# Kernel optimization log

Measured on AMD Instinct MI355X. Metric: run time of the kernel, lower is better.

Reference implementation:

```python
import jax, jax.numpy as jnp
import numpy as np

N, B, S, A, H, E = 8, 8192, 64, 16, 512, 4  # agents, batch, state, action, hidden, heads
D = H // E  # attend_dim


def setup_inputs() -> dict:
    key = jax.random.key(0)
    ks = jax.random.split(key, 12)
    g = lambda k, shape, fan: (jax.random.normal(k, shape, jnp.float32) / np.float32(np.sqrt(fan)))
    return {
        "states": jax.random.normal(ks[0], (N, B, S), jnp.float32),
        "actions": jax.random.normal(ks[1], (N, B, A), jnp.float32),
        # per-agent state encoder (Linear + LeakyReLU)
        "Ws": g(ks[2], (N, S, H), S), "bs": jnp.zeros((N, H), jnp.float32),
        # per-agent state-action encoder
        "Wsa": g(ks[3], (N, S + A, H), S + A), "bsa": jnp.zeros((N, H), jnp.float32),
        # shared per-head extractors (key/selector bias-free, value has bias+LeakyReLU)
        "Wk": g(ks[4], (E, H, D), H),
        "Wsel": g(ks[5], (E, H, D), H),
        "Wv": g(ks[6], (E, H, D), H), "bv": jnp.zeros((E, D), jnp.float32),
        # per-agent critic head (2H -> H -> 1)
        "Wc1": g(ks[7], (N, 2 * H, H), 2 * H), "bc1": jnp.zeros((N, H), jnp.float32),
        "Wc2": g(ks[8], (N, H, 1), H), "bc2": jnp.zeros((N, 1), jnp.float32),
        # per-agent value head (2H -> H -> 1)
        "Wv1": g(ks[9], (N, 2 * H, H), 2 * H), "bv1": jnp.zeros((N, H), jnp.float32),
        "Wv2": g(ks[10], (N, H, 1), H), "bv2": jnp.zeros((N, 1), jnp.float32),
    }


def reference(states, actions, Ws, bs, Wsa, bsa, Wk, Wsel, Wv, bv,
              Wc1, bc1, Wc2, bc2, Wv1, bv1, Wv2, bv2):
    lrelu = jax.nn.leaky_relu  # slope 0.01, matches nn.LeakyReLU default
    # encoders: [N,B,H]
    s_enc = lrelu(jnp.einsum('nbs,nsh->nbh', states, Ws) + bs[:, None, :])
    sa = jnp.concatenate([states, actions], axis=-1)
    sa_enc = lrelu(jnp.einsum('nbi,nih->nbh', sa, Wsa) + bsa[:, None, :])
    # per-head keys/selectors/values: [B,E,N,D]
    keys = jnp.einsum('nbh,ehd->bend', sa_enc, Wk)
    sels = jnp.einsum('nbh,ehd->bend', sa_enc, Wsel)
    vals = lrelu(jnp.einsum('nbh,ehd->bend', sa_enc, Wv) + bv[None, :, None, :])
    # each agent i attends over all agents j (including itself; no mask in source)
    logits = jnp.einsum('beid,bejd->beij', sels, keys) / jnp.float32(np.sqrt(D))
    weights = jax.nn.softmax(logits, axis=-1)
    other = jnp.einsum('beij,bejd->beid', weights, vals)  # [B,E,N,D]
    other = jnp.transpose(other, (2, 0, 1, 3)).reshape(N, B, H)  # heads concat -> [N,B,H]
    critic_in = jnp.concatenate([sa_enc, other], axis=-1)  # [N,B,2H]
    value_in = jnp.concatenate([s_enc, other], axis=-1)
    q = jnp.einsum('nbh,nho->nbo', lrelu(jnp.einsum('nbi,nih->nbh', critic_in, Wc1) + bc1[:, None, :]), Wc2) + bc2[:, None, :]
    v = jnp.einsum('nbh,nho->nbo', lrelu(jnp.einsum('nbi,nih->nbh', value_in, Wv1) + bv1[:, None, :]), Wv2) + bv2[:, None, :]
    return q, v  # each [N,B,1]
```

## Files before the change

### kernel.cpp

```cpp
#include <hip/hip_runtime.h>


#define DEVI __device__ __forceinline__

typedef unsigned short us16;
typedef __bf16 bf16x8 __attribute__((ext_vector_type(8)));
typedef float f32x4 __attribute__((ext_vector_type(4)));
typedef unsigned short u16x8 __attribute__((ext_vector_type(8)));

DEVI us16 f2bf(float f) {
  unsigned u = __builtin_bit_cast(unsigned, f);
  u += 0x7FFFu + ((u >> 16) & 1u);
  return (us16)(u >> 16);
}
DEVI float bf2f(us16 h) {
  unsigned u = ((unsigned)h) << 16;
  return __builtin_bit_cast(float, u);
}
DEVI float lrelu(float v) { return v > 0.f ? v : 0.01f * v; }
DEVI int pk2(float a, float b) { return (int)f2bf(a) | ((int)f2bf(b) << 16); }

DEVI void gload16(const us16* g, us16* l) {
  __builtin_amdgcn_global_load_lds(
      (const __attribute__((address_space(1))) void*)g,
      (__attribute__((address_space(3))) void*)l, 16, 0, 0);
}

__global__ void tconv_k(const float* __restrict__ src, long srcSlice, int K, int O,
                        us16* __restrict__ dst, long dstSlice, int dstRowOff,
                        int ldd, int Kpad)
{
  __shared__ float t[32][33];
  const int s = blockIdx.z;
  const int k0 = blockIdx.x * 32, o0 = blockIdx.y * 32;
  const int lx = threadIdx.x, ly = threadIdx.y;
#pragma unroll
  for (int i = 0; i < 4; i++) {
    int k = k0 + ly + i * 8, o = o0 + lx;
    float v = 0.f;
    if (k < K && o < O) v = src[(long)s * srcSlice + (long)k * O + o];
    t[ly + i * 8][lx] = v;
  }
  __syncthreads();
#pragma unroll
  for (int i = 0; i < 4; i++) {
    int o = o0 + ly + i * 8, k = k0 + lx;
    if (o < O && k < Kpad)
      dst[(long)s * dstSlice + (long)(dstRowOff + o) * ldd + k] = f2bf(t[lx][ly + i * 8]);
  }
}

enum { ASRC_F32 = 2, ASRC_F32_CAT = 3 };

template <int ASRC, int KTOT>
__global__ __launch_bounds__(256, 4)
void enc_gemm_k(const float* __restrict__ Ap, long aSlice,
                const float* __restrict__ A2p, long a2Slice,
                const us16* __restrict__ Btp, long bSlice,
                const float* __restrict__ bias, long biasSlice,
                us16* __restrict__ outB, long outSlice, long outRow)
{
  __shared__ us16 lA[128 * 32];
  __shared__ us16 lB[128 * 32];
  const int tid = threadIdx.x;
  const int z = blockIdx.z;
  const int m0 = blockIdx.x * 128;
  const int n0 = blockIdx.y * 128;
  const int wv = tid >> 6, lane = tid & 63;
  const int wm = (wv >> 1) * 64, wn = (wv & 1) * 64;
  const int fr = lane & 15, fk = (lane >> 4) * 8;
  const int rbase = (lane >> 4) * 4;
  const int grow = tid >> 2, gcol = (tid & 3) * 8;

  f32x4 acc[4][4];
#pragma unroll
  for (int i = 0; i < 4; i++)
#pragma unroll
    for (int j = 0; j < 4; j++) acc[i][j] = f32x4{0.f, 0.f, 0.f, 0.f};

  const us16* bbase = Btp + (long)z * bSlice + (long)n0 * KTOT;

  for (int k0 = 0; k0 < KTOT; k0 += 32) {
    int4 ra0, ra1;
    {
      const int srow = tid >> 1, scol0 = (tid & 1) * 16;
      const int kg = k0 + scol0;
      const float* a = nullptr;
      if constexpr (ASRC == ASRC_F32) {
        a = Ap + (long)z * aSlice + (long)(m0 + srow) * 64 + kg;
      } else {
        if (kg < 64)      a = Ap + (long)z * aSlice + (long)(m0 + srow) * 64 + kg;
        else if (kg < 80) a = A2p + (long)z * a2Slice + (long)(m0 + srow) * 16 + (kg - 64);
      }
      float4 f0, f1, f2, f3;
      if (a) { const float4* ap = (const float4*)a; f0 = ap[0]; f1 = ap[1]; f2 = ap[2]; f3 = ap[3]; }
      else   { f0 = make_float4(0.f, 0.f, 0.f, 0.f); f1 = f0; f2 = f0; f3 = f0; }
      ra0.x = pk2(f0.x, f0.y); ra0.y = pk2(f0.z, f0.w); ra0.z = pk2(f1.x, f1.y); ra0.w = pk2(f1.z, f1.w);
      ra1.x = pk2(f2.x, f2.y); ra1.y = pk2(f2.z, f2.w); ra1.z = pk2(f3.x, f3.y); ra1.w = pk2(f3.z, f3.w);
    }

    __syncthreads();
    {
      const us16* bb = bbase + k0 + gcol;
      gload16(bb + (long)grow * KTOT, &lB[tid * 8]);
      gload16(bb + (long)(64 + grow) * KTOT, &lB[2048 + tid * 8]);
    }
    {
      const int srow = tid >> 1, scol0 = (tid & 1) * 16;
      *(int4*)&lA[srow * 32 + scol0]     = ra0;
      *(int4*)&lA[srow * 32 + scol0 + 8] = ra1;
    }
    __syncthreads();

    bf16x8 af[4], bfg[4];
#pragma unroll
    for (int f = 0; f < 4; f++) af[f]  = *(const bf16x8*)&lA[(wm + f * 16 + fr) * 32 + fk];
#pragma unroll
    for (int f = 0; f < 4; f++) bfg[f] = *(const bf16x8*)&lB[(wn + f * 16 + fr) * 32 + fk];
#pragma unroll
    for (int fm = 0; fm < 4; fm++)
#pragma unroll
      for (int fn = 0; fn < 4; fn++)
        acc[fm][fn] = __builtin_amdgcn_mfma_f32_16x16x32_bf16(af[fm], bfg[fn], acc[fm][fn], 0, 0, 0);
  }

#pragma unroll
  for (int fm = 0; fm < 4; fm++) {
#pragma unroll
    for (int fn = 0; fn < 4; fn++) {
      int col = n0 + wn + fn * 16 + fr;
      float badd = bias[(long)z * biasSlice + col];
      us16* op = outB + (long)z * outSlice + (long)(m0 + wm + fm * 16 + rbase) * outRow + col;
#pragma unroll
      for (int j = 0; j < 4; j++) {
        float v = lrelu(acc[fm][fn][j] + badd);
        op[(long)j * outRow] = f2bf(v);
      }
    }
  }
}

enum { EPI_KSV = 1, EPI_DOT = 2 };

template <bool CAT, int EPI, int KTOT>
__global__ __launch_bounds__(256, 4)
void gemm64_k(const us16* __restrict__ Ap, long aSlice,
              const us16* __restrict__ A2p, long a2Slice,
              const us16* __restrict__ Btp, long bSlice,
              const float* __restrict__ bias,
              us16* __restrict__ outB, long outSlice, long outRow,
              const float* __restrict__ dotW, float* __restrict__ partial)
{
  __shared__ us16 lA[128 * 64];
  __shared__ us16 lB[128 * 64];
  const int tid = threadIdx.x;
  const int z = blockIdx.z;
  const int m0 = blockIdx.x * 128;
  const int n0 = blockIdx.y * 128;
  const int wv = tid >> 6, lane = tid & 63;
  const int wm = (wv >> 1) * 64, wn = (wv & 1) * 64;
  const int fr = lane & 15, fk = (lane >> 4) * 8;
  const int rbase = (lane >> 4) * 4;
  const int xorkey = (fr & 7) << 3;

  f32x4 acc[4][4];
#pragma unroll
  for (int i = 0; i < 4; i++)
#pragma unroll
    for (int j = 0; j < 4; j++) acc[i][j] = f32x4{0.f, 0.f, 0.f, 0.f};

  const us16* bbase = Btp + (long)z * bSlice + (long)n0 * KTOT;

  for (int k0 = 0; k0 < KTOT; k0 += 64) {
    __syncthreads();
#pragma unroll
    for (int i = 0; i < 4; i++) {
      const int c = i * 256 + tid;
      const int r = c >> 3;
      const int col = ((c & 7) ^ (r & 7)) << 3;
      const us16* a;
      if constexpr (!CAT) {
        a = Ap + (long)z * aSlice + (long)(m0 + r) * KTOT + (k0 + col);
      } else {
        const int kg = k0 + col;
        a = (kg < 512) ? Ap  + (long)z * aSlice  + (long)(m0 + r) * 512 + kg
                       : A2p + (long)z * a2Slice + (long)(m0 + r) * 512 + (kg - 512);
      }
      gload16(a, &lA[c * 8]);
    }
#pragma unroll
    for (int i = 0; i < 4; i++) {
      const int c = i * 256 + tid;
      const int r = c >> 3;
      const int col = ((c & 7) ^ (r & 7)) << 3;
      gload16(bbase + (long)r * KTOT + (k0 + col), &lB[c * 8]);
    }
    __syncthreads();

#pragma unroll
    for (int ks = 0; ks < 2; ks++) {
      bf16x8 af[4], bfg[4];
      const int kc = ks * 32 + fk;
#pragma unroll
      for (int f = 0; f < 4; f++)
        af[f]  = *(const bf16x8*)&lA[(wm + f * 16 + fr) * 64 + (kc ^ xorkey)];
#pragma unroll
      for (int f = 0; f < 4; f++)
        bfg[f] = *(const bf16x8*)&lB[(wn + f * 16 + fr) * 64 + (kc ^ xorkey)];
#pragma unroll
      for (int fm = 0; fm < 4; fm++)
#pragma unroll
        for (int fn = 0; fn < 4; fn++)
          acc[fm][fn] = __builtin_amdgcn_mfma_f32_16x16x32_bf16(af[fm], bfg[fn], acc[fm][fn], 0, 0, 0);
    }
  }

  if constexpr (EPI == EPI_DOT) {
    const float* bsl = bias + (long)z * 512;
    const float* wsl = dotW + (long)z * 512;
#pragma unroll
    for (int fm = 0; fm < 4; fm++) {
#pragma unroll
      for (int j = 0; j < 4; j++) {
        float p = 0.f;
#pragma unroll
        for (int fn = 0; fn < 4; fn++) {
          int col = n0 + wn + fn * 16 + fr;
          float v = acc[fm][fn][j] + bsl[col];
          v = lrelu(v);
          p += v * wsl[col];
        }
        p += __shfl_xor(p, 1); p += __shfl_xor(p, 2); p += __shfl_xor(p, 4); p += __shfl_xor(p, 8);
        if (fr == 0) {
          long row = (long)z * 8192 + (m0 + wm + fm * 16 + rbase + j);
          partial[row * 8 + blockIdx.y * 2 + (wv & 1)] = p;
        }
      }
    }
  } else {
#pragma unroll
    for (int fm = 0; fm < 4; fm++) {
#pragma unroll
      for (int fn = 0; fn < 4; fn++) {
        int col = n0 + wn + fn * 16 + fr;
        float badd = 0.f; bool act = false;
        if (col >= 256) { badd = bias[col - 256]; act = true; }
        us16* op = outB + (long)z * outSlice + (long)(m0 + wm + fm * 16 + rbase) * outRow + col;
#pragma unroll
        for (int j = 0; j < 4; j++) {
          float v = acc[fm][fn][j] + badd;
          if (act) v = lrelu(v);
          op[(long)j * outRow] = f2bf(v);
        }
      }
    }
  }
}

__global__ __launch_bounds__(256, 2)
void attn_k(const us16* __restrict__ ksv, us16* __restrict__ other, int e)
{
  __shared__ us16 t[4][8 * 392];
  const int wv = threadIdx.x >> 6, lane = threadIdx.x & 63;
  const long b = (long)blockIdx.x * 4 + wv;
  const us16* src = ksv + b * 3072;
#pragma unroll
  for (int i = 0; i < 6; i++) {
    int c = i * 64 + lane;
    int r = c / 48, cc = c - r * 48;
    *(int4*)&t[wv][r * 392 + cc * 8] = *(const int4*)&src[c * 8];
  }
  __syncthreads();
  const int i = lane >> 3, j = lane & 7;
  const us16* selp = &t[wv][i * 392 + 128];
  const us16* keyp = &t[wv][j * 392];
  float acc = 0.f;
#pragma unroll
  for (int d = 0; d < 128; d += 8) {
    u16x8 s8 = *(const u16x8*)&selp[d];
    u16x8 k8 = *(const u16x8*)&keyp[d];
#pragma unroll
    for (int q = 0; q < 8; q++) acc += bf2f(s8[q]) * bf2f(k8[q]);
  }
  acc *= 0.088388347648318447f;
  float mx = acc;
  mx = fmaxf(mx, __shfl_xor(mx, 1)); mx = fmaxf(mx, __shfl_xor(mx, 2)); mx = fmaxf(mx, __shfl_xor(mx, 4));
  float ex = __expf(acc - mx);
  float sm = ex;
  sm += __shfl_xor(sm, 1); sm += __shfl_xor(sm, 2); sm += __shfl_xor(sm, 4);
  float wsm = ex / sm;
  float wj[8];
  const int ibase = lane & 56;
#pragma unroll
  for (int jj = 0; jj < 8; jj++) wj[jj] = __shfl(wsm, ibase + jj);
  const int dbase = (lane & 7) * 16;
  float o[16];
#pragma unroll
  for (int q = 0; q < 16; q++) o[q] = 0.f;
#pragma unroll
  for (int jj = 0; jj < 8; jj++) {
    u16x8 v0 = *(const u16x8*)&t[wv][jj * 392 + 256 + dbase];
    u16x8 v1 = *(const u16x8*)&t[wv][jj * 392 + 256 + dbase + 8];
    float wgt = wj[jj];
#pragma unroll
    for (int q = 0; q < 8; q++) { o[q] += wgt * bf2f(v0[q]); o[8 + q] += wgt * bf2f(v1[q]); }
  }
  u16x8 r0, r1;
#pragma unroll
  for (int q = 0; q < 8; q++) { r0[q] = f2bf(o[q]); r1[q] = f2bf(o[8 + q]); }
  us16* dst = other + ((long)i * 8192 + b) * 512 + e * 128 + dbase;
  *(u16x8*)&dst[0] = r0;
  *(u16x8*)&dst[8] = r1;
}

__global__ void reduce_dot_k(const float* __restrict__ part, const float* __restrict__ b2,
                             float* __restrict__ out)
{
  int r = blockIdx.x * 256 + threadIdx.x;
  const float4* p = (const float4*)(part + (long)r * 8);
  float4 a = p[0], b = p[1];
  out[r] = b2[r >> 13] + ((a.x + a.y) + (a.z + a.w)) + ((b.x + b.y) + (b.z + b.w));
}

extern "C" void kernel_launch(void* const* d_in, const int* in_sizes, int n_in,
                              void* d_out, int out_size, void* d_ws, size_t ws_size,
                              hipStream_t stream)
{
  const float* states = (const float*)d_in[0];
  const float* actions= (const float*)d_in[1];
  const float* Ws  = (const float*)d_in[2];
  const float* bs  = (const float*)d_in[3];
  const float* Wsa = (const float*)d_in[4];
  const float* bsa = (const float*)d_in[5];
  const float* Wk  = (const float*)d_in[6];
  const float* Wsel= (const float*)d_in[7];
  const float* Wv  = (const float*)d_in[8];
  const float* bv  = (const float*)d_in[9];
  const float* Wc1 = (const float*)d_in[10];
  const float* bc1 = (const float*)d_in[11];
  const float* Wc2 = (const float*)d_in[12];
  const float* bc2 = (const float*)d_in[13];
  const float* Wv1 = (const float*)d_in[14];
  const float* bv1 = (const float*)d_in[15];
  const float* Wv2 = (const float*)d_in[16];
  const float* bv2 = (const float*)d_in[17];

  char* ws = (char*)d_ws;
  constexpr size_t OFF_WST   = 0;
  constexpr size_t OFF_WSAT  = OFF_WST   + (size_t)8 * 512 * 64 * 2;
  constexpr size_t OFF_WKVST = OFF_WSAT  + (size_t)8 * 512 * 96 * 2;
  constexpr size_t OFF_WC1T  = OFF_WKVST + (size_t)4 * 384 * 512 * 2;
  constexpr size_t OFF_WV1T  = OFF_WC1T  + (size_t)8 * 512 * 1024 * 2;
  constexpr size_t OFF_ENC   = OFF_WV1T  + (size_t)8 * 512 * 1024 * 2;
  constexpr size_t OFF_OTHER = OFF_ENC   + (size_t)8 * 8192 * 512 * 2;
  constexpr size_t OFF_KSV   = OFF_OTHER + (size_t)8 * 8192 * 512 * 2;
  constexpr size_t OFF_PART  = OFF_KSV   + (size_t)8192 * 8 * 384 * 2;
  constexpr size_t NEED      = OFF_PART  + (size_t)65536 * 8 * 4;
  if (ws_size < NEED) return;

  us16* WST   = (us16*)(ws + OFF_WST);
  us16* WSAT  = (us16*)(ws + OFF_WSAT);
  us16* WKVST = (us16*)(ws + OFF_WKVST);
  us16* WC1T  = (us16*)(ws + OFF_WC1T);
  us16* WV1T  = (us16*)(ws + OFF_WV1T);
  us16* ENC   = (us16*)(ws + OFF_ENC);
  us16* OTHER = (us16*)(ws + OFF_OTHER);
  us16* KSV   = (us16*)(ws + OFF_KSV);
  float* PART = (float*)(ws + OFF_PART);

  dim3 tb(32, 8);
  tconv_k<<<dim3(2, 16, 8),  tb, 0, stream>>>(Ws,  (long)64 * 512,  64,  512, WST,  (long)512 * 64,  0,   64,   64);
  tconv_k<<<dim3(3, 16, 8),  tb, 0, stream>>>(Wsa, (long)80 * 512,  80,  512, WSAT, (long)512 * 96,  0,   96,   96);
  tconv_k<<<dim3(16, 4, 4),  tb, 0, stream>>>(Wk,  (long)512 * 128, 512, 128, WKVST,(long)384 * 512, 0,   512,  512);
  tconv_k<<<dim3(16, 4, 4),  tb, 0, stream>>>(Wsel,(long)512 * 128, 512, 128, WKVST,(long)384 * 512, 128, 512,  512);
  tconv_k<<<dim3(16, 4, 4),  tb, 0, stream>>>(Wv,  (long)512 * 128, 512, 128, WKVST,(long)384 * 512, 256, 512,  512);
  tconv_k<<<dim3(32, 16, 8), tb, 0, stream>>>(Wc1, (long)1024 * 512,1024,512, WC1T, (long)512 * 1024,0,   1024, 1024);
  tconv_k<<<dim3(32, 16, 8), tb, 0, stream>>>(Wv1, (long)1024 * 512,1024,512, WV1T, (long)512 * 1024,0,   1024, 1024);

  enc_gemm_k<ASRC_F32_CAT, 96><<<dim3(64, 4, 8), 256, 0, stream>>>(
      states, (long)8192 * 64, actions, (long)8192 * 16, WSAT, (long)512 * 96, bsa, 512,
      ENC, (long)8192 * 512, 512);

  for (int e = 0; e < 4; e++) {
    gemm64_k<false, EPI_KSV, 512><<<dim3(64, 3, 8), 256, 0, stream>>>(
        ENC, (long)8192 * 512, nullptr, 0, WKVST + (size_t)e * 384 * 512, 0, bv + e * 128,
        KSV, 384, 3072, nullptr, nullptr);
    attn_k<<<dim3(2048), 256, 0, stream>>>(KSV, OTHER, e);
  }

  gemm64_k<true, EPI_DOT, 1024><<<dim3(64, 4, 8), 256, 0, stream>>>(
      ENC, (long)8192 * 512, OTHER, (long)8192 * 512, WC1T, (long)512 * 1024, bc1,
      nullptr, 0, 0, Wc2, PART);
  reduce_dot_k<<<dim3(256), 256, 0, stream>>>(PART, bc2, (float*)d_out);

  enc_gemm_k<ASRC_F32, 64><<<dim3(64, 4, 8), 256, 0, stream>>>(
      states, (long)8192 * 64, nullptr, 0, WST, (long)512 * 64, bs, 512,
      ENC, (long)8192 * 512, 512);

  gemm64_k<true, EPI_DOT, 1024><<<dim3(64, 4, 8), 256, 0, stream>>>(
      ENC, (long)8192 * 512, OTHER, (long)8192 * 512, WV1T, (long)512 * 1024, bv1,
      nullptr, 0, 0, Wv2, PART);
  reduce_dot_k<<<dim3(256), 256, 0, stream>>>(PART, bv2, (float*)d_out + 65536);
}
```

Baseline: 436.9 us.

## Double-buffer LDS tiles in the GEMM kernel to overlap loads with MFMA

Replaces the single-buffered GEMM main loop with a two-stage LDS ping-pong. The next K tile is prefetched via global_load_lds while MFMAs run on the current tile, gated by explicit vmcnt waits and raw s_barrier. Both LDS fragments are loaded before the MFMA burst, and wave priority is raised during the MFMAs. LDS per block doubles to 64 KB and launch bounds drop to 2 blocks per SIMD, trading occupancy for latency hiding.

New measurement: 458.9 us. 1.05x slower.

```diff
diff --git a/kernel.cpp b/kernel.cpp
--- a/kernel.cpp
+++ b/kernel.cpp
@@ -142,17 +142,46 @@
 
 enum { EPI_KSV = 1, EPI_DOT = 2 };
 
+template <bool CAT, int KTOT>
+DEVI void stage_tile(const us16* __restrict__ Ap, long aSlice,
+                     const us16* __restrict__ A2p, long a2Slice,
+                     const us16* __restrict__ bbase, int z, int m0, int k0,
+                     int tid, us16* ldsA, us16* ldsB)
+{
+#pragma unroll
+  for (int i = 0; i < 4; i++) {
+    const int c = i * 256 + tid;
+    const int r = c >> 3;
+    const int col = ((c & 7) ^ (r & 7)) << 3;
+    const us16* a;
+    if constexpr (!CAT) {
+      a = Ap + (long)z * aSlice + (long)(m0 + r) * KTOT + (k0 + col);
+    } else {
+      const int kg = k0 + col;
+      a = (kg < 512) ? Ap  + (long)z * aSlice  + (long)(m0 + r) * 512 + kg
+                     : A2p + (long)z * a2Slice + (long)(m0 + r) * 512 + (kg - 512);
+    }
+    gload16(a, ldsA + c * 8);
+  }
+#pragma unroll
+  for (int i = 0; i < 4; i++) {
+    const int c = i * 256 + tid;
+    const int r = c >> 3;
+    const int col = ((c & 7) ^ (r & 7)) << 3;
+    gload16(bbase + (long)r * KTOT + (k0 + col), ldsB + c * 8);
+  }
+}
+
 template <bool CAT, int EPI, int KTOT>
-__global__ __launch_bounds__(256, 4)
-void gemm64_k(const us16* __restrict__ Ap, long aSlice,
-              const us16* __restrict__ A2p, long a2Slice,
-              const us16* __restrict__ Btp, long bSlice,
-              const float* __restrict__ bias,
-              us16* __restrict__ outB, long outSlice, long outRow,
-              const float* __restrict__ dotW, float* __restrict__ partial)
-{
-  __shared__ us16 lA[128 * 64];
-  __shared__ us16 lB[128 * 64];
+__global__ __launch_bounds__(256, 2)
+void gemm64db_k(const us16* __restrict__ Ap, long aSlice,
+                const us16* __restrict__ A2p, long a2Slice,
+                const us16* __restrict__ Btp, long bSlice,
+                const float* __restrict__ bias,
+                us16* __restrict__ outB, long outSlice, long outRow,
+                const float* __restrict__ dotW, float* __restrict__ partial)
+{
+  __shared__ us16 lds[2][2][128 * 64];
   const int tid = threadIdx.x;
   const int z = blockIdx.z;
   const int m0 = blockIdx.x * 128;
@@ -171,48 +200,47 @@
 
   const us16* bbase = Btp + (long)z * bSlice + (long)n0 * KTOT;
 
-  for (int k0 = 0; k0 < KTOT; k0 += 64) {
-    __syncthreads();
-#pragma unroll
-    for (int i = 0; i < 4; i++) {
-      const int c = i * 256 + tid;
-      const int r = c >> 3;
-      const int col = ((c & 7) ^ (r & 7)) << 3;
-      const us16* a;
-      if constexpr (!CAT) {
-        a = Ap + (long)z * aSlice + (long)(m0 + r) * KTOT + (k0 + col);
-      } else {
-        const int kg = k0 + col;
-        a = (kg < 512) ? Ap  + (long)z * aSlice  + (long)(m0 + r) * 512 + kg
-                       : A2p + (long)z * a2Slice + (long)(m0 + r) * 512 + (kg - 512);
-      }
-      gload16(a, &lA[c * 8]);
-    }
-#pragma unroll
-    for (int i = 0; i < 4; i++) {
-      const int c = i * 256 + tid;
-      const int r = c >> 3;
-      const int col = ((c & 7) ^ (r & 7)) << 3;
-      gload16(bbase + (long)r * KTOT + (k0 + col), &lB[c * 8]);
-    }
-    __syncthreads();
-
+  constexpr int NT = KTOT / 64;
+  stage_tile<CAT, KTOT>(Ap, aSlice, A2p, a2Slice, bbase, z, m0, 0, tid,
+                        &lds[0][0][0], &lds[0][1][0]);
+
+#pragma unroll 2
+  for (int t = 0; t < NT; ++t) {
+    const int d = t & 1;
+    if (t + 1 < NT) {
+      stage_tile<CAT, KTOT>(Ap, aSlice, A2p, a2Slice, bbase, z, m0, (t + 1) * 64,
+                            tid, &lds[d ^ 1][0][0], &lds[d ^ 1][1][0]);
+      asm volatile("s_waitcnt vmcnt(8)" ::: "memory");
+    } else {
+      asm volatile("s_waitcnt vmcnt(0)" ::: "memory");
+    }
+    __builtin_amdgcn_s_barrier();
+    __builtin_amdgcn_sched_barrier(0);
+
+    const us16* la = &lds[d][0][0];
+    const us16* lb = &lds[d][1][0];
+    bf16x8 af[2][4], bfg[2][4];
 #pragma unroll
     for (int ks = 0; ks < 2; ks++) {
-      bf16x8 af[4], bfg[4];
       const int kc = ks * 32 + fk;
 #pragma unroll
       for (int f = 0; f < 4; f++)
-        af[f]  = *(const bf16x8*)&lA[(wm + f * 16 + fr) * 64 + (kc ^ xorkey)];
+        af[ks][f]  = *(const bf16x8*)&la[(wm + f * 16 + fr) * 64 + (kc ^ xorkey)];
 #pragma unroll
       for (int f = 0; f < 4; f++)
-        bfg[f] = *(const bf16x8*)&lB[(wn + f * 16 + fr) * 64 + (kc ^ xorkey)];
+        bfg[ks][f] = *(const bf16x8*)&lb[(wn + f * 16 + fr) * 64 + (kc ^ xorkey)];
+    }
+    __builtin_amdgcn_s_setprio(1);
+#pragma unroll
+    for (int ks = 0; ks < 2; ks++)
 #pragma unroll
       for (int fm = 0; fm < 4; fm++)
 #pragma unroll
         for (int fn = 0; fn < 4; fn++)
-          acc[fm][fn] = __builtin_amdgcn_mfma_f32_16x16x32_bf16(af[fm], bfg[fn], acc[fm][fn], 0, 0, 0);
-    }
+          acc[fm][fn] = __builtin_amdgcn_mfma_f32_16x16x32_bf16(af[ks][fm], bfg[ks][fn], acc[fm][fn], 0, 0, 0);
+    __builtin_amdgcn_s_setprio(0);
+    __builtin_amdgcn_s_barrier();
+    __builtin_amdgcn_sched_barrier(0);
   }
 
   if constexpr (EPI == EPI_DOT) {
@@ -382,13 +410,13 @@
       ENC, (long)8192 * 512, 512);
 
   for (int e = 0; e < 4; e++) {
-    gemm64_k<false, EPI_KSV, 512><<<dim3(64, 3, 8), 256, 0, stream>>>(
+    gemm64db_k<false, EPI_KSV, 512><<<dim3(64, 3, 8), 256, 0, stream>>>(
         ENC, (long)8192 * 512, nullptr, 0, WKVST + (size_t)e * 384 * 512, 0, bv + e * 128,
         KSV, 384, 3072, nullptr, nullptr);
     attn_k<<<dim3(2048), 256, 0, stream>>>(KSV, OTHER, e);
   }
 
-  gemm64_k<true, EPI_DOT, 1024><<<dim3(64, 4, 8), 256, 0, stream>>>(
+  gemm64db_k<true, EPI_DOT, 1024><<<dim3(64, 4, 8), 256, 0, stream>>>(
       ENC, (long)8192 * 512, OTHER, (long)8192 * 512, WC1T, (long)512 * 1024, bc1,
       nullptr, 0, 0, Wc2, PART);
   reduce_dot_k<<<dim3(256), 256, 0, stream>>>(PART, bc2, (float*)d_out);
@@ -397,7 +425,7 @@
       states, (long)8192 * 64, nullptr, 0, WST, (long)512 * 64, bs, 512,
       ENC, (long)8192 * 512, 512);
 
-  gemm64_k<true, EPI_DOT, 1024><<<dim3(64, 4, 8), 256, 0, stream>>>(
+  gemm64db_k<true, EPI_DOT, 1024><<<dim3(64, 4, 8), 256, 0, stream>>>(
       ENC, (long)8192 * 512, OTHER, (long)8192 * 512, WV1T, (long)512 * 1024, bv1,
       nullptr, 0, 0, Wv2, PART);
   reduce_dot_k<<<dim3(256), 256, 0, stream>>>(PART, bv2, (float*)d_out + 65536);
```
